# Performance work log

Hardware: AMD Instinct MI355X
Metric: run time of the kernel (lower is better)

The kernel has to match this reference:

```python
import jax, jax.numpy as jnp
import numpy as np

NUM_EXPERTS = 8
TOP_K = 2
LORA_ALPHA = 2.0
LORA_RANK = 16
D_MODEL = 2048
D_HIDDEN = 5632


def setup_inputs() -> dict:
    key = jax.random.key(0)
    ks = jax.random.split(key, 11)
    B, S, D, H, E, R = 2, 1024, D_MODEL, D_HIDDEN, NUM_EXPERTS, LORA_RANK
    sd = 1.0 / np.sqrt(D)
    sh = 1.0 / np.sqrt(H)
    x = jax.random.normal(ks[0], (B, S, D), jnp.float32)
    gate_w = jax.random.normal(ks[1], (E, D), jnp.float32) * sd   # router Linear(D->E), no bias
    w_up = jax.random.normal(ks[2], (H, D), jnp.float32) * sd     # up_proj.weight
    w_gate = jax.random.normal(ks[3], (H, D), jnp.float32) * sd   # gate_proj.weight
    w_down = jax.random.normal(ks[4], (D, H), jnp.float32) * sh   # down_proj.weight
    up_A = jax.random.normal(ks[5], (E, R, D), jnp.float32) * sd
    up_B = jax.random.normal(ks[6], (E, H, R), jnp.float32) * 0.02
    gate_A = jax.random.normal(ks[7], (E, R, D), jnp.float32) * sd
    gate_B = jax.random.normal(ks[8], (E, H, R), jnp.float32) * 0.02
    down_A = jax.random.normal(ks[9], (E, R, H), jnp.float32) * sh
    down_B = jax.random.normal(ks[10], (E, D, R), jnp.float32) * 0.02
    return {"x": x, "gate_w": gate_w, "w_up": w_up, "w_gate": w_gate,
            "w_down": w_down, "up_A": up_A, "up_B": up_B,
            "gate_A": gate_A, "gate_B": gate_B, "down_A": down_A, "down_B": down_B}


def reference(x, gate_w, w_up, w_gate, w_down, up_A, up_B, gate_A, gate_B, down_A, down_B):
    B, S, D = x.shape
    H = w_up.shape[0]
    # router: logits [B,S,E], top-k over experts (last dim)
    gate_logits = jnp.einsum('bsd,ed->bse', x, gate_w)
    topw, sel = jax.lax.top_k(gate_logits, TOP_K)            # [B,S,k]
    # NOTE: source applies softmax over dim=1 (the SEQUENCE axis) -- reproduced faithfully
    topw = jax.nn.softmax(topw.astype(jnp.float32), axis=1).astype(x.dtype)
    xt = x.reshape(-1, D)                                    # [T, D]
    wf = topw.reshape(-1, TOP_K)                             # [T, k]
    sf = sel.reshape(-1, TOP_K)                              # [T, k]
    # shared base projections computed once for all tokens
    base_up = xt @ w_up.T                                    # [T, H]
    base_gate = xt @ w_gate.T                                # [T, H]
    mixed_h = jnp.zeros((xt.shape[0], H), x.dtype)
    lora_down = jnp.zeros_like(xt)
    # loop over fixed small expert count; low-rank LoRA deltas applied without
    # materializing full merged weights (same math by linearity of matmul)
    for e in range(NUM_EXPERTS):
        c = jnp.sum(jnp.where(sf == e, wf, 0.0), axis=1)     # [T] routing weight (0 if not routed)
        lo_up = LORA_ALPHA * ((xt @ up_A[e].T) @ up_B[e].T)
        lo_gate = LORA_ALPHA * ((xt @ gate_A[e].T) @ gate_B[e].T)
        h_e = jax.nn.silu(base_up + lo_up) * (base_gate + lo_gate)  # [T, H]
        ch = c[:, None] * h_e
        mixed_h = mixed_h + ch
        lora_down = lora_down + LORA_ALPHA * ((ch @ down_A[e].T) @ down_B[e].T)
    out = mixed_h @ w_down.T + lora_down                     # base down GEMM done once on mixed hidden
    return out.reshape(B, S, D)
```

## Files before the change

kernel.cpp:

```cpp
#include <hip/hip_runtime.h>
#include <hip/hip_fp16.h>
#include <cmath>

#define TOKENS 2048
#define DMODEL 2048
#define DHID   5632
#define NEXP   8
#define RANK   16
#define LALPHA 2.0f

typedef __attribute__((ext_vector_type(4))) float f32x4;
typedef __attribute__((ext_vector_type(8))) short s16x8;
typedef __attribute__((ext_vector_type(4))) short s16x4;
typedef __attribute__((ext_vector_type(8))) _Float16 f16x8;

__device__ __forceinline__ short f2bf(float f){
  unsigned u = __float_as_uint(f);
  u += 0x7fffu + ((u >> 16) & 1u);
  return (short)(u >> 16);
}
__device__ __forceinline__ short f2h(float f){
  return (short)__half_as_ushort(__float2half(f));
}

struct Stage { const short* s0; const short* s1; short* d0; short* d1; };

__device__ __forceinline__ Stage mk_stage(const short* g, long ld, short* t, int tid){
  Stage st;
  const int L0 = tid,      r0 = L0>>2, c0 = ((L0&3) - (r0>>1)) & 3;
  const int L1 = 256+tid,  r1 = L1>>2, c1 = ((L1&3) - (r1>>1)) & 3;
  st.s0 = g + (long)r0*ld + c0*8;  st.d0 = t + L0*8;
  st.s1 = g + (long)r1*ld + c1*8;  st.d1 = t + L1*8;
  return st;
}
__device__ __forceinline__ void do_stage(const Stage& st, int k0){
  __builtin_amdgcn_global_load_lds((const __attribute__((address_space(1))) void*)(st.s0 + k0),
                                   (__attribute__((address_space(3))) void*)st.d0, 16, 0, 0);
  __builtin_amdgcn_global_load_lds((const __attribute__((address_space(1))) void*)(st.s1 + k0),
                                   (__attribute__((address_space(3))) void*)st.d1, 16, 0, 0);
}
__device__ __forceinline__ s16x8 fragb(const short* t, int row, int quad){
  const int p = (quad + (row>>1)) & 3;
  return *(const s16x8*)(t + (row*4 + p)*8);
}
__device__ __forceinline__ f16x8 fragh(const short* t, int row, int quad){
  const int p = (quad + (row>>1)) & 3;
  return *(const f16x8*)(t + (row*4 + p)*8);
}

__global__ void k_cast(const float* __restrict__ x, const float* __restrict__ w_up,
                       const float* __restrict__ w_gate, const float* __restrict__ w_down,
                       const float* __restrict__ upA, const float* __restrict__ gateA,
                       const float* __restrict__ downA, const float* __restrict__ upB,
                       const float* __restrict__ gateB, const float* __restrict__ downB,
                       short* __restrict__ xb, short* __restrict__ wub, short* __restrict__ wgb,
                       short* __restrict__ wdb, short* __restrict__ daA, short* __restrict__ acat,
                       short* __restrict__ upBcat, short* __restrict__ gateBcat, short* __restrict__ wdbcat){
  const long e0 = 4194304, e1 = 15728640, e2 = 27262976, e3 = 38797312;
  const long e4 = 39518208, e5 = 40042496, e6 = 40763392, e7 = 41484288, e8 = 41746432;
  const long i = ((long)blockIdx.x*256 + threadIdx.x) * 4;
  if(i >= e8) return;
  const float* src; short* dst; long l; int fp16 = 0;
  if(i < e0){ src = x; dst = xb; l = i; }
  else if(i < e1){ src = w_up; dst = wub; l = i - e0; }
  else if(i < e2){ src = w_gate; dst = wgb; l = i - e1; }
  else if(i < e3){ src = w_down; dst = wdb; l = i - e2; }
  else if(i < e4){ src = downA; dst = daA; l = i - e3; }
  else if(i < e5){
    l = i - e4;
    const long c = l>>11;
    const long e = c>>5, pj = (c>>4)&1, r = c&15;
    src = (pj ? gateA : upA) + ((e*RANK + r)<<11) + (l&2047) - l;
    dst = acat;
  }
  else if(i < e6){
    l = i - e5;
    const long h = l>>7, c = l&127, e = c>>4, r = c&15;
    src = upB + ((e*DHID + h)*RANK + r) - l;
    dst = upBcat; fp16 = 1;
  }
  else if(i < e7){
    l = i - e6;
    const long h = l>>7, c = l&127, e = c>>4, r = c&15;
    src = gateB + ((e*DHID + h)*RANK + r) - l;
    dst = gateBcat; fp16 = 1;
  }
  else {
    l = i - e7;
    const long d = l>>7, c = l&127, e = c>>4, r = c&15;
    src = downB + ((e*DMODEL + d)*RANK + r) - l;
    dst = wdbcat; fp16 = 1;
  }
  const float4 v = *(const float4*)(src + l);
  s16x4 o;
  if(fp16){ o[0]=f2h(v.x); o[1]=f2h(v.y); o[2]=f2h(v.z); o[3]=f2h(v.w); }
  else    { o[0]=f2bf(v.x); o[1]=f2bf(v.y); o[2]=f2bf(v.z); o[3]=f2bf(v.w); }
  *(s16x4*)(dst + l) = o;
}

__global__ void k_router(const float* __restrict__ x, const float* __restrict__ gw,
                         int* __restrict__ sel, float* __restrict__ topv){
  const int t = blockIdx.x*4 + (threadIdx.x>>6);
  const int lane = threadIdx.x & 63;
  const float* xr = x + (long)t * DMODEL;
  float acc[NEXP];
  #pragma unroll
  for(int e=0;e<NEXP;e++) acc[e]=0.f;
  #pragma unroll
  for(int it=0; it<8; it++){
    const int d = it*256 + lane*4;
    const float4 xv = *(const float4*)(xr + d);
    #pragma unroll
    for(int e=0;e<NEXP;e++){
      const float4 wv = *(const float4*)(gw + e*DMODEL + d);
      acc[e] += xv.x*wv.x + xv.y*wv.y + xv.z*wv.z + xv.w*wv.w;
    }
  }
  #pragma unroll
  for(int e=0;e<NEXP;e++){
    #pragma unroll
    for(int off=32; off; off>>=1) acc[e] += __shfl_down(acc[e], off, 64);
  }
  if(lane==0){
    int i0=0;
    #pragma unroll
    for(int e=1;e<NEXP;e++) if(acc[e]>acc[i0]) i0=e;
    int i1=-1;
    #pragma unroll
    for(int e=0;e<NEXP;e++){ if(e==i0) continue; if(i1<0 || acc[e]>acc[i1]) i1=e; }
    sel[t*2+0]=i0; sel[t*2+1]=i1;
    topv[t*2+0]=acc[i0]; topv[t*2+1]=acc[i1];
  }
}

__global__ void k_softmax(const float* __restrict__ topv, float* __restrict__ cw){
  const int b = blockIdx.x >> 1, k = blockIdx.x & 1;
  const int base = b*1024;
  __shared__ float red[256];
  float v[4];
  float mx = -1e30f;
  #pragma unroll
  for(int i=0;i<4;i++){
    int s = threadIdx.x + i*256;
    v[i] = topv[(base+s)*2 + k];
    mx = fmaxf(mx, v[i]);
  }
  red[threadIdx.x]=mx; __syncthreads();
  for(int o=128;o;o>>=1){ if(threadIdx.x<o) red[threadIdx.x]=fmaxf(red[threadIdx.x],red[threadIdx.x+o]); __syncthreads(); }
  mx = red[0]; __syncthreads();
  float sum=0.f;
  #pragma unroll
  for(int i=0;i<4;i++){ v[i]=__expf(v[i]-mx); sum+=v[i]; }
  red[threadIdx.x]=sum; __syncthreads();
  for(int o=128;o;o>>=1){ if(threadIdx.x<o) red[threadIdx.x]+=red[threadIdx.x+o]; __syncthreads(); }
  const float inv = 1.f/red[0];
  #pragma unroll
  for(int i=0;i<4;i++){
    int s = threadIdx.x + i*256;
    cw[(base+s)*2+k] = v[i]*inv;
  }
}

__global__ __launch_bounds__(256,3) void k_rank(
    const short* __restrict__ xb, const short* __restrict__ acat, float* __restrict__ Rall){
  __shared__ __align__(16) short At[4096];
  __shared__ __align__(16) short Bt[4096];
  const int c0 = blockIdx.x*128, t0 = blockIdx.y*128;
  const int tid = threadIdx.x, lane = tid&63, wave = tid>>6;
  const int wm=(wave>>1)*64, wn=(wave&1)*64, fr=lane&15, quad=lane>>4;
  f32x4 acc[4][4];
  #pragma unroll
  for(int i=0;i<4;i++)
    #pragma unroll
    for(int j=0;j<4;j++) acc[i][j]=(f32x4){0.f,0.f,0.f,0.f};
  const Stage sA = mk_stage(xb + (long)t0*DMODEL, DMODEL, At, tid);
  const Stage sB = mk_stage(acat + (long)c0*DMODEL, DMODEL, Bt, tid);
  for(int k0=0; k0<DMODEL; k0+=32){
    do_stage(sA, k0); do_stage(sB, k0);
    __syncthreads();
    s16x8 af[4];
    #pragma unroll
    for(int i=0;i<4;i++) af[i] = fragb(At, wm + i*16 + fr, quad);
    #pragma unroll
    for(int j=0;j<4;j++){
      const s16x8 bf = fragb(Bt, wn + j*16 + fr, quad);
      #pragma unroll
      for(int i=0;i<4;i++)
        acc[i][j] = __builtin_amdgcn_mfma_f32_16x16x32_bf16(af[i], bf, acc[i][j], 0,0,0);
    }
    __syncthreads();
  }
  #pragma unroll
  for(int i=0;i<4;i++)
    #pragma unroll
    for(int j=0;j<4;j++){
      const int rbase = wm + i*16 + quad*4, col = wn + j*16 + fr;
      #pragma unroll
      for(int reg=0;reg<4;reg++)
        Rall[(long)(t0+rbase+reg)*256 + c0 + col] = acc[i][j][reg];
    }
}

__global__ void k_rsel(const float* __restrict__ Rall, const int* __restrict__ sel,
                       short* __restrict__ RselU, short* __restrict__ RselG){
  const int idx = blockIdx.x*256 + threadIdx.x;
  const int c = idx & 127, t = (idx>>7) & (TOKENS-1), k = idx>>18;
  const int e = c>>4, r = c&15;
  const int s = sel[t*2+k];
  const int m = (e==s);
  RselU[idx] = f2h(m ? LALPHA*Rall[(long)t*256 + e*32 + r]      : 0.f);
  RselG[idx] = f2h(m ? LALPHA*Rall[(long)t*256 + e*32 + 16 + r] : 0.f);
}

__global__ __launch_bounds__(256,2) void k_lora(
    const short* __restrict__ RselU, const short* __restrict__ RselG,
    const short* __restrict__ upBcat, const short* __restrict__ gateBcat,
    __half* __restrict__ LU, __half* __restrict__ LG){
  __shared__ __align__(16) short At[4096];
  __shared__ __align__(16) short Gt[4096];
  __shared__ __align__(16) short Bt[4096];
  const int h0 = blockIdx.x*128, t0 = blockIdx.y*128;
  const short* Rsel = blockIdx.z ? RselG : RselU;
  const short* Bcat = blockIdx.z ? gateBcat : upBcat;
  __half* Lout      = blockIdx.z ? LG : LU;
  const int tid = threadIdx.x, lane = tid&63, wave = tid>>6;
  const int wm=(wave>>1)*64, wn=(wave&1)*64, fr=lane&15, quad=lane>>4;
  f32x4 l0[4][4], l1[4][4];
  #pragma unroll
  for(int i=0;i<4;i++)
    #pragma unroll
    for(int j=0;j<4;j++){ l0[i][j]=(f32x4){0.f,0.f,0.f,0.f}; l1[i][j]=l0[i][j]; }
  const Stage sB  = mk_stage(Bcat + (long)h0*128, 128, Bt, tid);
  const Stage sR0 = mk_stage(Rsel + (long)t0*128, 128, At, tid);
  const Stage sR1 = mk_stage(Rsel + ((long)TOKENS + t0)*128, 128, Gt, tid);
  for(int k0=0; k0<128; k0+=32){
    do_stage(sB, k0); do_stage(sR0, k0); do_stage(sR1, k0);
    __syncthreads();
    f16x8 a0[4], a1[4];
    #pragma unroll
    for(int i=0;i<4;i++){ a0[i] = fragh(At, wm + i*16 + fr, quad); a1[i] = fragh(Gt, wm + i*16 + fr, quad); }
    #pragma unroll
    for(int j=0;j<4;j++){
      const f16x8 bf = fragh(Bt, wn + j*16 + fr, quad);
      #pragma unroll
      for(int i=0;i<4;i++){
        l0[i][j] = __builtin_amdgcn_mfma_f32_16x16x32_f16(a0[i], bf, l0[i][j], 0,0,0);
        l1[i][j] = __builtin_amdgcn_mfma_f32_16x16x32_f16(a1[i], bf, l1[i][j], 0,0,0);
      }
    }
    __syncthreads();
  }
  #pragma unroll
  for(int i=0;i<4;i++)
    #pragma unroll
    for(int j=0;j<4;j++){
      const int rbase = wm + i*16 + quad*4, col = wn + j*16 + fr;
      #pragma unroll
      for(int reg=0;reg<4;reg++){
        LoopStore:;
        Lout[((long)(t0+rbase+reg))*DHID + h0 + col]          = __float2half(l0[i][j][reg]);
        Lout[((long)TOKENS + t0+rbase+reg)*DHID + h0 + col]   = __float2half(l1[i][j][reg]);
      }
    }
}

__global__ __launch_bounds__(256,2) void k_main(
    const short* __restrict__ xb, const short* __restrict__ wub, const short* __restrict__ wgb,
    const __half* __restrict__ LU, const __half* __restrict__ LG,
    const float* __restrict__ cw, unsigned short* __restrict__ ch, unsigned short* __restrict__ chsum){
  __shared__ __align__(16) short At[4096];
  __shared__ __align__(16) short Ut[4096];
  __shared__ __align__(16) short Gt[4096];
  __shared__ float cwv[128][2];
  const int h0 = blockIdx.x*128, t0 = blockIdx.y*128;
  const int tid = threadIdx.x, lane = tid&63, wave = tid>>6;
  const int wm=(wave>>1)*64, wn=(wave&1)*64, fr=lane&15, quad=lane>>4;
  if(tid < 256){ const int tl = tid>>1, k = tid&1; cwv[tl][k] = cw[(t0+tl)*2 + k]; }
  f32x4 au[4][4], ag[4][4];
  #pragma unroll
  for(int i=0;i<4;i++)
    #pragma unroll
    for(int j=0;j<4;j++){ au[i][j]=(f32x4){0.f,0.f,0.f,0.f}; ag[i][j]=au[i][j]; }
  const Stage sA = mk_stage(xb + (long)t0*DMODEL, DMODEL, At, tid);
  const Stage sU = mk_stage(wub + (long)h0*DMODEL, DMODEL, Ut, tid);
  const Stage sG = mk_stage(wgb + (long)h0*DMODEL, DMODEL, Gt, tid);
  for(int k0=0; k0<DMODEL; k0+=32){
    do_stage(sA, k0); do_stage(sU, k0); do_stage(sG, k0);
    __syncthreads();
    s16x8 af[4];
    #pragma unroll
    for(int i=0;i<4;i++) af[i] = fragb(At, wm + i*16 + fr, quad);
    #pragma unroll
    for(int j=0;j<4;j++){
      const s16x8 bu = fragb(Ut, wn + j*16 + fr, quad);
      const s16x8 bg = fragb(Gt, wn + j*16 + fr, quad);
      #pragma unroll
      for(int i=0;i<4;i++){
        au[i][j] = __builtin_amdgcn_mfma_f32_16x16x32_bf16(af[i], bu, au[i][j], 0,0,0);
        ag[i][j] = __builtin_amdgcn_mfma_f32_16x16x32_bf16(af[i], bg, ag[i][j], 0,0,0);
      }
    }
    __syncthreads();
  }
  #pragma unroll
  for(int i=0;i<4;i++){
    #pragma unroll
    for(int reg=0;reg<4;reg++){
      const int tl = wm + i*16 + quad*4 + reg;
      const float c0 = cwv[tl][0], c1 = cwv[tl][1];
      const long row0 = (long)(t0+tl)*DHID + h0;
      const long row1 = ((long)TOKENS + t0+tl)*DHID + h0;
      const __half* pu0 = LU + row0; const __half* pu1 = LU + row1;
      const __half* pg0 = LG + row0; const __half* pg1 = LG + row1;
      unsigned short* r0 = ch + row0;
      unsigned short* r1 = ch + row1;
      unsigned short* rs = chsum + row0;
      #pragma unroll
      for(int j=0;j<4;j++){
        const int hl = wn + j*16 + fr;
        const float u0 = au[i][j][reg] + __half2float(pu0[hl]);
        const float g0 = ag[i][j][reg] + __half2float(pg0[hl]);
        const float h0v = (u0 / (1.f + __expf(-u0))) * g0;
        const float u1 = au[i][j][reg] + __half2float(pu1[hl]);
        const float g1 = ag[i][j][reg] + __half2float(pg1[hl]);
        const float h1v = (u1 / (1.f + __expf(-u1))) * g1;
        const float v0 = c0*h0v, v1 = c1*h1v;
        r0[hl] = (unsigned short)f2bf(v0);
        r1[hl] = (unsigned short)f2bf(v1);
        rs[hl] = (unsigned short)f2bf(v0+v1);
      }
    }
  }
}

__global__ __launch_bounds__(256,4) void k_rd(
    const unsigned short* __restrict__ ch, const short* __restrict__ daA,
    float* __restrict__ RD){
  __shared__ __align__(16) short At[4096];
  __shared__ __align__(16) short Bt[4096];
  const int slot = blockIdx.x>>4, ks = blockIdx.x&15;
  const int t0 = blockIdx.y*128;
  const int tid = threadIdx.x, lane = tid&63, wave = tid>>6;
  const int wm=(wave>>1)*64, wn=(wave&1)*64, fr=lane&15, quad=lane>>4;
  f32x4 acc[4][4];
  #pragma unroll
  for(int i=0;i<4;i++)
    #pragma unroll
    for(int j=0;j<4;j++) acc[i][j]=(f32x4){0.f,0.f,0.f,0.f};
  const Stage sA = mk_stage((const short*)ch + ((long)slot*TOKENS + t0)*DHID, DHID, At, tid);
  const Stage sB = mk_stage(daA, DHID, Bt, tid);
  const int kbeg = ks*352;
  for(int kk=0; kk<352; kk+=32){
    do_stage(sA, kbeg+kk); do_stage(sB, kbeg+kk);
    __syncthreads();
    s16x8 af[4];
    #pragma unroll
    for(int i=0;i<4;i++) af[i] = fragb(At, wm + i*16 + fr, quad);
    #pragma unroll
    for(int j=0;j<4;j++){
      const s16x8 bf = fragb(Bt, wn + j*16 + fr, quad);
      #pragma unroll
      for(int i=0;i<4;i++)
        acc[i][j] = __builtin_amdgcn_mfma_f32_16x16x32_bf16(af[i], bf, acc[i][j], 0,0,0);
    }
    __syncthreads();
  }
  #pragma unroll
  for(int i=0;i<4;i++)
    #pragma unroll
    for(int j=0;j<4;j++){
      const int rbase = wm + i*16 + quad*4, col = wn + j*16 + fr;
      #pragma unroll
      for(int reg=0;reg<4;reg++)
        atomicAdd(&RD[((long)(t0+rbase+reg)*2 + slot)*128 + col], acc[i][j][reg]);
    }
}

__global__ void k_scatter(const float* __restrict__ RD, const int* __restrict__ sel,
                          __half* __restrict__ RDhat){
  const int idx = blockIdx.x*256 + threadIdx.x;
  const int t = idx>>7, c = idx&127, e = c>>4;
  const int s0 = sel[t*2], s1 = sel[t*2+1];
  float v = 0.f;
  if(e == s0) v = LALPHA * RD[((long)t*2+0)*128 + c];
  else if(e == s1) v = LALPHA * RD[((long)t*2+1)*128 + c];
  RDhat[idx] = __float2half(v);
}

__global__ __launch_bounds__(256,4) void k_down(
    const unsigned short* __restrict__ chsum, const short* __restrict__ wdb,
    const short* __restrict__ RDhat, const short* __restrict__ wdbcat,
    float* __restrict__ out){
  __shared__ __align__(16) short At[4096];
  __shared__ __align__(16) short Bt[4096];
  const int d0 = blockIdx.x*128, t0 = blockIdx.y*128, ks = blockIdx.z;
  const int tid = threadIdx.x, lane = tid&63, wave = tid>>6;
  const int wm=(wave>>1)*64, wn=(wave&1)*64, fr=lane&15, quad=lane>>4;
  f32x4 acc[4][4];
  #pragma unroll
  for(int i=0;i<4;i++)
    #pragma unroll
    for(int j=0;j<4;j++) acc[i][j]=(f32x4){0.f,0.f,0.f,0.f};
  const Stage sA = mk_stage((const short*)chsum + (long)t0*DHID, DHID, At, tid);
  const Stage sB = mk_stage(wdb + (long)d0*DHID, DHID, Bt, tid);
  const int kbeg = ks*2816;
  for(int kk=0; kk<2816; kk+=32){
    do_stage(sA, kbeg+kk); do_stage(sB, kbeg+kk);
    __syncthreads();
    s16x8 af[4];
    #pragma unroll
    for(int i=0;i<4;i++) af[i] = fragb(At, wm + i*16 + fr, quad);
    #pragma unroll
    for(int j=0;j<4;j++){
      const s16x8 bf = fragb(Bt, wn + j*16 + fr, quad);
      #pragma unroll
      for(int i=0;i<4;i++)
        acc[i][j] = __builtin_amdgcn_mfma_f32_16x16x32_bf16(af[i], bf, acc[i][j], 0,0,0);
    }
    __syncthreads();
  }
  if(ks == 0){
    const Stage sAh = mk_stage(RDhat + (long)t0*128, 128, At, tid);
    const Stage sBh = mk_stage(wdbcat + (long)d0*128, 128, Bt, tid);
    for(int k0=0; k0<128; k0+=32){
      do_stage(sAh, k0); do_stage(sBh, k0);
      __syncthreads();
      f16x8 af[4];
      #pragma unroll
      for(int i=0;i<4;i++) af[i] = fragh(At, wm + i*16 + fr, quad);
      #pragma unroll
      for(int j=0;j<4;j++){
        const f16x8 bf = fragh(Bt, wn + j*16 + fr, quad);
        #pragma unroll
        for(int i=0;i<4;i++)
          acc[i][j] = __builtin_amdgcn_mfma_f32_16x16x32_f16(af[i], bf, acc[i][j], 0,0,0);
      }
      __syncthreads();
    }
  }
  #pragma unroll
  for(int i=0;i<4;i++)
    #pragma unroll
    for(int j=0;j<4;j++){
      const int rbase = wm + i*16 + quad*4, col = wn + j*16 + fr;
      #pragma unroll
      for(int reg=0;reg<4;reg++)
        atomicAdd(&out[(long)(t0+rbase+reg)*DMODEL + d0 + col], acc[i][j][reg]);
    }
}

extern "C" void kernel_launch(void* const* d_in, const int* in_sizes, int n_in,
                              void* d_out, int out_size, void* d_ws, size_t ws_size,
                              hipStream_t stream){
  (void)in_sizes; (void)n_in; (void)out_size; (void)ws_size;
  const float* x      = (const float*)d_in[0];
  const float* gate_w = (const float*)d_in[1];
  const float* w_up   = (const float*)d_in[2];
  const float* w_gate = (const float*)d_in[3];
  const float* w_down = (const float*)d_in[4];
  const float* up_A   = (const float*)d_in[5];
  const float* up_B   = (const float*)d_in[6];
  const float* gate_A = (const float*)d_in[7];
  const float* gate_B = (const float*)d_in[8];
  const float* down_A = (const float*)d_in[9];
  const float* down_B = (const float*)d_in[10];
  float* out = (float*)d_out;

  char* ws = (char*)d_ws;
  size_t off = 0;
  auto alloc = [&](size_t bytes){ void* p = ws + off; off += (bytes + 255) & ~(size_t)255; return p; };
  short* xb       = (short*)alloc((size_t)TOKENS*DMODEL*2);
  short* wub      = (short*)alloc((size_t)DHID*DMODEL*2);
  short* wgb      = (short*)alloc((size_t)DHID*DMODEL*2);
  short* wdb      = (short*)alloc((size_t)DMODEL*DHID*2);
  short* daA      = (short*)alloc((size_t)128*DHID*2);
  short* acat     = (short*)alloc((size_t)256*DMODEL*2);
  short* upBcat   = (short*)alloc((size_t)DHID*128*2);
  short* gateBcat = (short*)alloc((size_t)DHID*128*2);
  short* wdbcat   = (short*)alloc((size_t)DMODEL*128*2);
  unsigned short* ch    = (unsigned short*)alloc((size_t)2*TOKENS*DHID*2);
  unsigned short* chsum = (unsigned short*)alloc((size_t)TOKENS*DHID*2);
  __half* LU    = (__half*)alloc((size_t)2*TOKENS*DHID*2);
  __half* LG    = (__half*)alloc((size_t)2*TOKENS*DHID*2);
  float* Rall   = (float*)alloc((size_t)TOKENS*256*4);
  short* RselU  = (short*)alloc((size_t)2*TOKENS*128*2);
  short* RselG  = (short*)alloc((size_t)2*TOKENS*128*2);
  float* RD     = (float*)alloc((size_t)TOKENS*2*128*4);
  __half* RDhat = (__half*)alloc((size_t)TOKENS*128*2);
  int*   sel    = (int*)alloc((size_t)TOKENS*2*4);
  float* topv   = (float*)alloc((size_t)TOKENS*2*4);
  float* cw     = (float*)alloc((size_t)TOKENS*2*4);

  (void)hipMemsetAsync(RD, 0, (size_t)TOKENS*2*128*4, stream);
  (void)hipMemsetAsync(out, 0, (size_t)TOKENS*DMODEL*4, stream);
  k_cast<<<40768, 256, 0, stream>>>(x, w_up, w_gate, w_down, up_A, gate_A, down_A,
                                    up_B, gate_B, down_B,
                                    xb, wub, wgb, wdb, daA, acat, upBcat, gateBcat, wdbcat);
  k_router<<<512, 256, 0, stream>>>(x, gate_w, sel, topv);
  k_softmax<<<4, 256, 0, stream>>>(topv, cw);
  k_rank<<<dim3(2,16), 256, 0, stream>>>(xb, acat, Rall);
  k_rsel<<<2048, 256, 0, stream>>>(Rall, sel, RselU, RselG);
  k_lora<<<dim3(44,16,2), 256, 0, stream>>>(RselU, RselG, upBcat, gateBcat, LU, LG);
  k_main<<<dim3(44,16), 256, 0, stream>>>(xb, wub, wgb, LU, LG, cw, ch, chsum);
  k_rd<<<dim3(32,16), 256, 0, stream>>>(ch, daA, RD);
  k_scatter<<<1024, 256, 0, stream>>>(RD, sel, RDhat);
  k_down<<<dim3(16,16,2), 256, 0, stream>>>(chsum, wdb, (const short*)RDhat, wdbcat, out);
}
```

Baseline: 585.1 us.

## Use 64-wide K tiles, split-K rank GEMM, and fragment-ordered LoRA buffer

All GEMM kernels move from 32-wide to 64-wide K staging with an 8-way XOR-swizzled LDS layout. This halves the number of barrier-separated iterations at the cost of more LDS per block and lower launch-bound occupancy. The rank GEMM is split 8 ways over K with atomic accumulation into a zeroed Rall buffer, which raises its block count from 32 to 256. The LoRA up/gate outputs are stored in a per-thread fragment-ordered layout with vector stores, so k_main reads them as contiguous 16-byte loads instead of scattered half loads.

Measured after the change: 581.9 us. Within noise of the previous version (-0.5%).

```diff
diff --git a/kernel.cpp b/kernel.cpp
--- a/kernel.cpp
+++ b/kernel.cpp
@@ -43,9 +43,37 @@
   const int p = (quad + (row>>1)) & 3;
   return *(const s16x8*)(t + (row*4 + p)*8);
 }
-__device__ __forceinline__ f16x8 fragh(const short* t, int row, int quad){
-  const int p = (quad + (row>>1)) & 3;
-  return *(const f16x8*)(t + (row*4 + p)*8);
+
+struct Stage64 { const short* g; short* t; int off[4]; int dof; };
+
+__device__ __forceinline__ Stage64 mk_stage64(const short* g, long ld, short* t, int tid){
+  Stage64 st; st.g = g; st.t = t;
+  #pragma unroll
+  for(int p=0;p<4;p++){
+    const int L = p*256 + tid;
+    const int r = L>>3, cp = L&7;
+    const int c = (cp - (r&7)) & 7;
+    st.off[p] = r*(int)ld + c*8;
+  }
+  st.dof = tid*8;
+  return st;
+}
+__device__ __forceinline__ void do_stage64(const Stage64& st, int k0){
+  #pragma unroll
+  for(int p=0;p<4;p++)
+    __builtin_amdgcn_global_load_lds(
+      (const __attribute__((address_space(1))) void*)(st.g + st.off[p] + k0),
+      (__attribute__((address_space(3))) void*)(st.t + st.dof + p*2048), 16, 0, 0);
+}
+__device__ __forceinline__ s16x8 fragb64(const short* t, int row, int ksub, int quad){
+  const int c = ksub*4 + quad;
+  const int p = (c + (row&7)) & 7;
+  return *(const s16x8*)(t + (row*8 + p)*8);
+}
+__device__ __forceinline__ f16x8 fragh64(const short* t, int row, int ksub, int quad){
+  const int c = ksub*4 + quad;
+  const int p = (c + (row&7)) & 7;
+  return *(const f16x8*)(t + (row*8 + p)*8);
 }
 
 __global__ void k_cast(const float* __restrict__ x, const float* __restrict__ w_up,
@@ -161,11 +189,12 @@
   }
 }
 
-__global__ __launch_bounds__(256,3) void k_rank(
+__global__ __launch_bounds__(256,2) void k_rank(
     const short* __restrict__ xb, const short* __restrict__ acat, float* __restrict__ Rall){
-  __shared__ __align__(16) short At[4096];
-  __shared__ __align__(16) short Bt[4096];
+  __shared__ __align__(16) short At[8192];
+  __shared__ __align__(16) short Bt[8192];
   const int c0 = blockIdx.x*128, t0 = blockIdx.y*128;
+  const int kbeg = blockIdx.z*256;
   const int tid = threadIdx.x, lane = tid&63, wave = tid>>6;
   const int wm=(wave>>1)*64, wn=(wave&1)*64, fr=lane&15, quad=lane>>4;
   f32x4 acc[4][4];
@@ -173,20 +202,23 @@
   for(int i=0;i<4;i++)
     #pragma unroll
     for(int j=0;j<4;j++) acc[i][j]=(f32x4){0.f,0.f,0.f,0.f};
-  const Stage sA = mk_stage(xb + (long)t0*DMODEL, DMODEL, At, tid);
-  const Stage sB = mk_stage(acat + (long)c0*DMODEL, DMODEL, Bt, tid);
-  for(int k0=0; k0<DMODEL; k0+=32){
-    do_stage(sA, k0); do_stage(sB, k0);
-    __syncthreads();
-    s16x8 af[4];
-    #pragma unroll
-    for(int i=0;i<4;i++) af[i] = fragb(At, wm + i*16 + fr, quad);
-    #pragma unroll
-    for(int j=0;j<4;j++){
-      const s16x8 bf = fragb(Bt, wn + j*16 + fr, quad);
-      #pragma unroll
-      for(int i=0;i<4;i++)
-        acc[i][j] = __builtin_amdgcn_mfma_f32_16x16x32_bf16(af[i], bf, acc[i][j], 0,0,0);
+  const Stage64 sA = mk_stage64(xb + (long)t0*DMODEL, DMODEL, At, tid);
+  const Stage64 sB = mk_stage64(acat + (long)c0*DMODEL, DMODEL, Bt, tid);
+  for(int k0=kbeg; k0<kbeg+256; k0+=64){
+    do_stage64(sA, k0); do_stage64(sB, k0);
+    __syncthreads();
+    #pragma unroll
+    for(int s=0;s<2;s++){
+      s16x8 af[4];
+      #pragma unroll
+      for(int i=0;i<4;i++) af[i] = fragb64(At, wm + i*16 + fr, s, quad);
+      #pragma unroll
+      for(int j=0;j<4;j++){
+        const s16x8 bf = fragb64(Bt, wn + j*16 + fr, s, quad);
+        #pragma unroll
+        for(int i=0;i<4;i++)
+          acc[i][j] = __builtin_amdgcn_mfma_f32_16x16x32_bf16(af[i], bf, acc[i][j], 0,0,0);
+      }
     }
     __syncthreads();
   }
@@ -197,7 +229,7 @@
       const int rbase = wm + i*16 + quad*4, col = wn + j*16 + fr;
       #pragma unroll
       for(int reg=0;reg<4;reg++)
-        Rall[(long)(t0+rbase+reg)*256 + c0 + col] = acc[i][j][reg];
+        atomicAdd(&Rall[(long)(t0+rbase+reg)*256 + c0 + col], acc[i][j][reg]);
     }
 }
 
@@ -215,14 +247,13 @@
 __global__ __launch_bounds__(256,2) void k_lora(
     const short* __restrict__ RselU, const short* __restrict__ RselG,
     const short* __restrict__ upBcat, const short* __restrict__ gateBcat,
-    __half* __restrict__ LU, __half* __restrict__ LG){
-  __shared__ __align__(16) short At[4096];
-  __shared__ __align__(16) short Gt[4096];
-  __shared__ __align__(16) short Bt[4096];
+    short* __restrict__ LF){
+  __shared__ __align__(16) short At[8192];
+  __shared__ __align__(16) short Gt[8192];
+  __shared__ __align__(16) short Bt[8192];
   const int h0 = blockIdx.x*128, t0 = blockIdx.y*128;
   const short* Rsel = blockIdx.z ? RselG : RselU;
   const short* Bcat = blockIdx.z ? gateBcat : upBcat;
-  __half* Lout      = blockIdx.z ? LG : LU;
   const int tid = threadIdx.x, lane = tid&63, wave = tid>>6;
   const int wm=(wave>>1)*64, wn=(wave&1)*64, fr=lane&15, quad=lane>>4;
   f32x4 l0[4][4], l1[4][4];
@@ -230,99 +261,115 @@
   for(int i=0;i<4;i++)
     #pragma unroll
     for(int j=0;j<4;j++){ l0[i][j]=(f32x4){0.f,0.f,0.f,0.f}; l1[i][j]=l0[i][j]; }
-  const Stage sB  = mk_stage(Bcat + (long)h0*128, 128, Bt, tid);
-  const Stage sR0 = mk_stage(Rsel + (long)t0*128, 128, At, tid);
-  const Stage sR1 = mk_stage(Rsel + ((long)TOKENS + t0)*128, 128, Gt, tid);
-  for(int k0=0; k0<128; k0+=32){
-    do_stage(sB, k0); do_stage(sR0, k0); do_stage(sR1, k0);
-    __syncthreads();
-    f16x8 a0[4], a1[4];
-    #pragma unroll
-    for(int i=0;i<4;i++){ a0[i] = fragh(At, wm + i*16 + fr, quad); a1[i] = fragh(Gt, wm + i*16 + fr, quad); }
-    #pragma unroll
-    for(int j=0;j<4;j++){
-      const f16x8 bf = fragh(Bt, wn + j*16 + fr, quad);
-      #pragma unroll
-      for(int i=0;i<4;i++){
-        l0[i][j] = __builtin_amdgcn_mfma_f32_16x16x32_f16(a0[i], bf, l0[i][j], 0,0,0);
-        l1[i][j] = __builtin_amdgcn_mfma_f32_16x16x32_f16(a1[i], bf, l1[i][j], 0,0,0);
+  const Stage64 sB  = mk_stage64(Bcat + (long)h0*128, 128, Bt, tid);
+  const Stage64 sR0 = mk_stage64(Rsel + (long)t0*128, 128, At, tid);
+  const Stage64 sR1 = mk_stage64(Rsel + ((long)TOKENS + t0)*128, 128, Gt, tid);
+  for(int k0=0; k0<128; k0+=64){
+    do_stage64(sB, k0); do_stage64(sR0, k0); do_stage64(sR1, k0);
+    __syncthreads();
+    #pragma unroll
+    for(int s=0;s<2;s++){
+      f16x8 a0[4], a1[4];
+      #pragma unroll
+      for(int i=0;i<4;i++){ a0[i] = fragh64(At, wm + i*16 + fr, s, quad);
+                            a1[i] = fragh64(Gt, wm + i*16 + fr, s, quad); }
+      #pragma unroll
+      for(int j=0;j<4;j++){
+        const f16x8 bf = fragh64(Bt, wn + j*16 + fr, s, quad);
+        #pragma unroll
+        for(int i=0;i<4;i++){
+          l0[i][j] = __builtin_amdgcn_mfma_f32_16x16x32_f16(a0[i], bf, l0[i][j], 0,0,0);
+          l1[i][j] = __builtin_amdgcn_mfma_f32_16x16x32_f16(a1[i], bf, l1[i][j], 0,0,0);
+        }
       }
     }
     __syncthreads();
   }
-  #pragma unroll
-  for(int i=0;i<4;i++)
-    #pragma unroll
-    for(int j=0;j<4;j++){
-      const int rbase = wm + i*16 + quad*4, col = wn + j*16 + fr;
-      #pragma unroll
-      for(int reg=0;reg<4;reg++){
-        LoopStore:;
-        Lout[((long)(t0+rbase+reg))*DHID + h0 + col]          = __float2half(l0[i][j][reg]);
-        Lout[((long)TOKENS + t0+rbase+reg)*DHID + h0 + col]   = __float2half(l1[i][j][reg]);
-      }
-    }
+  short* o = LF + (((long)(blockIdx.y*44 + blockIdx.x)*256 + tid)*256) + blockIdx.z*128;
+  #pragma unroll
+  for(int i=0;i<4;i++){
+    s16x8 p0a, p0b, p1a, p1b;
+    #pragma unroll
+    for(int r=0;r<4;r++){
+      p0a[r]   = f2h(l0[i][0][r]); p0a[4+r] = f2h(l0[i][1][r]);
+      p0b[r]   = f2h(l0[i][2][r]); p0b[4+r] = f2h(l0[i][3][r]);
+      p1a[r]   = f2h(l1[i][0][r]); p1a[4+r] = f2h(l1[i][1][r]);
+      p1b[r]   = f2h(l1[i][2][r]); p1b[4+r] = f2h(l1[i][3][r]);
+    }
+    *(s16x8*)(o + i*16)          = p0a;
+    *(s16x8*)(o + i*16 + 8)      = p0b;
+    *(s16x8*)(o + 64 + i*16)     = p1a;
+    *(s16x8*)(o + 64 + i*16 + 8) = p1b;
+  }
 }
 
 __global__ __launch_bounds__(256,2) void k_main(
     const short* __restrict__ xb, const short* __restrict__ wub, const short* __restrict__ wgb,
-    const __half* __restrict__ LU, const __half* __restrict__ LG,
+    const short* __restrict__ LF,
     const float* __restrict__ cw, unsigned short* __restrict__ ch, unsigned short* __restrict__ chsum){
-  __shared__ __align__(16) short At[4096];
-  __shared__ __align__(16) short Ut[4096];
-  __shared__ __align__(16) short Gt[4096];
+  __shared__ __align__(16) short At[8192];
+  __shared__ __align__(16) short Ut[8192];
+  __shared__ __align__(16) short Gt[8192];
   __shared__ float cwv[128][2];
   const int h0 = blockIdx.x*128, t0 = blockIdx.y*128;
   const int tid = threadIdx.x, lane = tid&63, wave = tid>>6;
   const int wm=(wave>>1)*64, wn=(wave&1)*64, fr=lane&15, quad=lane>>4;
-  if(tid < 256){ const int tl = tid>>1, k = tid&1; cwv[tl][k] = cw[(t0+tl)*2 + k]; }
+  { const int tl = tid>>1, k = tid&1; cwv[tl][k] = cw[(t0+tl)*2 + k]; }
   f32x4 au[4][4], ag[4][4];
   #pragma unroll
   for(int i=0;i<4;i++)
     #pragma unroll
     for(int j=0;j<4;j++){ au[i][j]=(f32x4){0.f,0.f,0.f,0.f}; ag[i][j]=au[i][j]; }
-  const Stage sA = mk_stage(xb + (long)t0*DMODEL, DMODEL, At, tid);
-  const Stage sU = mk_stage(wub + (long)h0*DMODEL, DMODEL, Ut, tid);
-  const Stage sG = mk_stage(wgb + (long)h0*DMODEL, DMODEL, Gt, tid);
-  for(int k0=0; k0<DMODEL; k0+=32){
-    do_stage(sA, k0); do_stage(sU, k0); do_stage(sG, k0);
-    __syncthreads();
-    s16x8 af[4];
-    #pragma unroll
-    for(int i=0;i<4;i++) af[i] = fragb(At, wm + i*16 + fr, quad);
-    #pragma unroll
-    for(int j=0;j<4;j++){
-      const s16x8 bu = fragb(Ut, wn + j*16 + fr, quad);
-      const s16x8 bg = fragb(Gt, wn + j*16 + fr, quad);
-      #pragma unroll
-      for(int i=0;i<4;i++){
-        au[i][j] = __builtin_amdgcn_mfma_f32_16x16x32_bf16(af[i], bu, au[i][j], 0,0,0);
-        ag[i][j] = __builtin_amdgcn_mfma_f32_16x16x32_bf16(af[i], bg, ag[i][j], 0,0,0);
+  const Stage64 sA = mk_stage64(xb + (long)t0*DMODEL, DMODEL, At, tid);
+  const Stage64 sU = mk_stage64(wub + (long)h0*DMODEL, DMODEL, Ut, tid);
+  const Stage64 sG = mk_stage64(wgb + (long)h0*DMODEL, DMODEL, Gt, tid);
+  for(int k0=0; k0<DMODEL; k0+=64){
+    do_stage64(sA, k0); do_stage64(sU, k0); do_stage64(sG, k0);
+    __syncthreads();
+    #pragma unroll
+    for(int s=0;s<2;s++){
+      s16x8 af[4];
+      #pragma unroll
+      for(int i=0;i<4;i++) af[i] = fragb64(At, wm + i*16 + fr, s, quad);
+      #pragma unroll
+      for(int j=0;j<4;j++){
+        const s16x8 bu = fragb64(Ut, wn + j*16 + fr, s, quad);
+        const s16x8 bg = fragb64(Gt, wn + j*16 + fr, s, quad);
+        #pragma unroll
+        for(int i=0;i<4;i++){
+          au[i][j] = __builtin_amdgcn_mfma_f32_16x16x32_bf16(af[i], bu, au[i][j], 0,0,0);
+          ag[i][j] = __builtin_amdgcn_mfma_f32_16x16x32_bf16(af[i], bg, ag[i][j], 0,0,0);
+        }
       }
     }
     __syncthreads();
   }
+  const short* Lf = LF + (((long)(blockIdx.y*44 + blockIdx.x)*256 + tid)*256);
   #pragma unroll
   for(int i=0;i<4;i++){
+    f16x8 Uv0[2], Uv1[2], Gv0[2], Gv1[2];
+    Uv0[0] = *(const f16x8*)(Lf + i*16);        Uv0[1] = *(const f16x8*)(Lf + i*16 + 8);
+    Uv1[0] = *(const f16x8*)(Lf + 64 + i*16);   Uv1[1] = *(const f16x8*)(Lf + 64 + i*16 + 8);
+    Gv0[0] = *(const f16x8*)(Lf + 128 + i*16);  Gv0[1] = *(const f16x8*)(Lf + 128 + i*16 + 8);
+    Gv1[0] = *(const f16x8*)(Lf + 192 + i*16);  Gv1[1] = *(const f16x8*)(Lf + 192 + i*16 + 8);
     #pragma unroll
     for(int reg=0;reg<4;reg++){
       const int tl = wm + i*16 + quad*4 + reg;
       const float c0 = cwv[tl][0], c1 = cwv[tl][1];
       const long row0 = (long)(t0+tl)*DHID + h0;
       const long row1 = ((long)TOKENS + t0+tl)*DHID + h0;
-      const __half* pu0 = LU + row0; const __half* pu1 = LU + row1;
-      const __half* pg0 = LG + row0; const __half* pg1 = LG + row1;
       unsigned short* r0 = ch + row0;
       unsigned short* r1 = ch + row1;
       unsigned short* rs = chsum + row0;
       #pragma unroll
       for(int j=0;j<4;j++){
         const int hl = wn + j*16 + fr;
-        const float u0 = au[i][j][reg] + __half2float(pu0[hl]);
-        const float g0 = ag[i][j][reg] + __half2float(pg0[hl]);
+        const int q = (j&1)*4 + reg, hv = j>>1;
+        const float u0 = au[i][j][reg] + (float)Uv0[hv][q];
+        const float g0 = ag[i][j][reg] + (float)Gv0[hv][q];
         const float h0v = (u0 / (1.f + __expf(-u0))) * g0;
-        const float u1 = au[i][j][reg] + __half2float(pu1[hl]);
-        const float g1 = ag[i][j][reg] + __half2float(pg1[hl]);
+        const float u1 = au[i][j][reg] + (float)Uv1[hv][q];
+        const float g1 = ag[i][j][reg] + (float)Gv1[hv][q];
         const float h1v = (u1 / (1.f + __expf(-u1))) * g1;
         const float v0 = c0*h0v, v1 = c1*h1v;
         r0[hl] = (unsigned short)f2bf(v0);
@@ -387,12 +434,12 @@
   RDhat[idx] = __float2half(v);
 }
 
-__global__ __launch_bounds__(256,4) void k_down(
+__global__ __launch_bounds__(256,2) void k_down(
     const unsigned short* __restrict__ chsum, const short* __restrict__ wdb,
     const short* __restrict__ RDhat, const short* __restrict__ wdbcat,
     float* __restrict__ out){
-  __shared__ __align__(16) short At[4096];
-  __shared__ __align__(16) short Bt[4096];
+  __shared__ __align__(16) short At[8192];
+  __shared__ __align__(16) short Bt[8192];
   const int d0 = blockIdx.x*128, t0 = blockIdx.y*128, ks = blockIdx.z;
   const int tid = threadIdx.x, lane = tid&63, wave = tid>>6;
   const int wm=(wave>>1)*64, wn=(wave&1)*64, fr=lane&15, quad=lane>>4;
@@ -401,39 +448,45 @@
   for(int i=0;i<4;i++)
     #pragma unroll
     for(int j=0;j<4;j++) acc[i][j]=(f32x4){0.f,0.f,0.f,0.f};
-  const Stage sA = mk_stage((const short*)chsum + (long)t0*DHID, DHID, At, tid);
-  const Stage sB = mk_stage(wdb + (long)d0*DHID, DHID, Bt, tid);
+  const Stage64 sA = mk_stage64((const short*)chsum + (long)t0*DHID, DHID, At, tid);
+  const Stage64 sB = mk_stage64(wdb + (long)d0*DHID, DHID, Bt, tid);
   const int kbeg = ks*2816;
-  for(int kk=0; kk<2816; kk+=32){
-    do_stage(sA, kbeg+kk); do_stage(sB, kbeg+kk);
-    __syncthreads();
-    s16x8 af[4];
-    #pragma unroll
-    for(int i=0;i<4;i++) af[i] = fragb(At, wm + i*16 + fr, quad);
-    #pragma unroll
-    for(int j=0;j<4;j++){
-      const s16x8 bf = fragb(Bt, wn + j*16 + fr, quad);
-      #pragma unroll
-      for(int i=0;i<4;i++)
-        acc[i][j] = __builtin_amdgcn_mfma_f32_16x16x32_bf16(af[i], bf, acc[i][j], 0,0,0);
-    }
-    __syncthreads();
-  }
-  if(ks == 0){
-    const Stage sAh = mk_stage(RDhat + (long)t0*128, 128, At, tid);
-    const Stage sBh = mk_stage(wdbcat + (long)d0*128, 128, Bt, tid);
-    for(int k0=0; k0<128; k0+=32){
-      do_stage(sAh, k0); do_stage(sBh, k0);
-      __syncthreads();
-      f16x8 af[4];
-      #pragma unroll
-      for(int i=0;i<4;i++) af[i] = fragh(At, wm + i*16 + fr, quad);
+  for(int kk=0; kk<2816; kk+=64){
+    do_stage64(sA, kbeg+kk); do_stage64(sB, kbeg+kk);
+    __syncthreads();
+    #pragma unroll
+    for(int s=0;s<2;s++){
+      s16x8 af[4];
+      #pragma unroll
+      for(int i=0;i<4;i++) af[i] = fragb64(At, wm + i*16 + fr, s, quad);
       #pragma unroll
       for(int j=0;j<4;j++){
-        const f16x8 bf = fragh(Bt, wn + j*16 + fr, quad);
+        const s16x8 bf = fragb64(Bt, wn + j*16 + fr, s, quad);
         #pragma unroll
         for(int i=0;i<4;i++)
-          acc[i][j] = __builtin_amdgcn_mfma_f32_16x16x32_f16(af[i], bf, acc[i][j], 0,0,0);
+          acc[i][j] = __builtin_amdgcn_mfma_f32_16x16x32_bf16(af[i], bf, acc[i][j], 0,0,0);
+      }
+    }
+    __syncthreads();
+  }
+  if(ks == 0){
+    const Stage64 sAh = mk_stage64(RDhat + (long)t0*128, 128, At, tid);
+    const Stage64 sBh = mk_stage64(wdbcat + (long)d0*128, 128, Bt, tid);
+    for(int k0=0; k0<128; k0+=64){
+      do_stage64(sAh, k0); do_stage64(sBh, k0);
+      __syncthreads();
+      #pragma unroll
+      for(int s=0;s<2;s++){
+        f16x8 af[4];
+        #pragma unroll
+        for(int i=0;i<4;i++) af[i] = fragh64(At, wm + i*16 + fr, s, quad);
+        #pragma unroll
+        for(int j=0;j<4;j++){
+          const f16x8 bf = fragh64(Bt, wn + j*16 + fr, s, quad);
+          #pragma unroll
+          for(int i=0;i<4;i++)
+            acc[i][j] = __builtin_amdgcn_mfma_f32_16x16x32_f16(af[i], bf, acc[i][j], 0,0,0);
+        }
       }
       __syncthreads();
     }
@@ -480,8 +533,7 @@
   short* wdbcat   = (short*)alloc((size_t)DMODEL*128*2);
   unsigned short* ch    = (unsigned short*)alloc((size_t)2*TOKENS*DHID*2);
   unsigned short* chsum = (unsigned short*)alloc((size_t)TOKENS*DHID*2);
-  __half* LU    = (__half*)alloc((size_t)2*TOKENS*DHID*2);
-  __half* LG    = (__half*)alloc((size_t)2*TOKENS*DHID*2);
+  short* LF     = (short*)alloc((size_t)704*256*256*2);
   float* Rall   = (float*)alloc((size_t)TOKENS*256*4);
   short* RselU  = (short*)alloc((size_t)2*TOKENS*128*2);
   short* RselG  = (short*)alloc((size_t)2*TOKENS*128*2);
@@ -492,16 +544,17 @@
   float* cw     = (float*)alloc((size_t)TOKENS*2*4);
 
   (void)hipMemsetAsync(RD, 0, (size_t)TOKENS*2*128*4, stream);
+  (void)hipMemsetAsync(Rall, 0, (size_t)TOKENS*256*4, stream);
   (void)hipMemsetAsync(out, 0, (size_t)TOKENS*DMODEL*4, stream);
   k_cast<<<40768, 256, 0, stream>>>(x, w_up, w_gate, w_down, up_A, gate_A, down_A,
                                     up_B, gate_B, down_B,
                                     xb, wub, wgb, wdb, daA, acat, upBcat, gateBcat, wdbcat);
   k_router<<<512, 256, 0, stream>>>(x, gate_w, sel, topv);
   k_softmax<<<4, 256, 0, stream>>>(topv, cw);
-  k_rank<<<dim3(2,16), 256, 0, stream>>>(xb, acat, Rall);
+  k_rank<<<dim3(2,16,8), 256, 0, stream>>>(xb, acat, Rall);
   k_rsel<<<2048, 256, 0, stream>>>(Rall, sel, RselU, RselG);
-  k_lora<<<dim3(44,16,2), 256, 0, stream>>>(RselU, RselG, upBcat, gateBcat, LU, LG);
-  k_main<<<dim3(44,16), 256, 0, stream>>>(xb, wub, wgb, LU, LG, cw, ch, chsum);
+  k_lora<<<dim3(44,16,2), 256, 0, stream>>>(RselU, RselG, upBcat, gateBcat, LF);
+  k_main<<<dim3(44,16), 256, 0, stream>>>(xb, wub, wgb, LF, cw, ch, chsum);
   k_rd<<<dim3(32,16), 256, 0, stream>>>(ch, daA, RD);
   k_scatter<<<1024, 256, 0, stream>>>(RD, sel, RDhat);
   k_down<<<dim3(16,16,2), 256, 0, stream>>>(chsum, wdb, (const short*)RDhat, wdbcat, out);
```
